# Kernel optimization log

Measured on AMD Instinct MI355X. Metric: run time of the kernel, lower is better.

The kernel has to match this reference:

```python
import jax, jax.numpy as jnp
import numpy as np
from jax import lax

B, C, H, W = 32, 3, 128, 128
S = 10             # max_segments
L = 200            # base_traj_length
TOTAL_LIMIT = 200  # traj_length (must equal L per original sample())
DOF = 2
HID = 2048
CONV_OUT = 512 * 6 * 6  # 128->126->63->61->30->28->14->12->6


def _conv(x, w, b):
    y = lax.conv_general_dilated(x, w, (1, 1), 'VALID', dimension_numbers=('NCHW', 'OIHW', 'NCHW'))
    return y + b[None, :, None, None]


def _pool_relu(x):
    return jax.nn.relu(lax.reduce_window(x, -jnp.inf, lax.max, (1, 1, 2, 2), (1, 1, 2, 2), 'VALID'))


def _rotate2d(y, y0, rot):
    # rotate points y (B,L,2) around per-batch center y0 (B,2) by rot (B,1,1) radians
    px, py = y[..., 0:1], y[..., 1:2]
    cx, cy = y0[:, 0][:, None, None], y0[:, 1][:, None, None]
    c, s = jnp.cos(rot), jnp.sin(rot)
    return jnp.concatenate([c * (px - cx) - s * (py - cy) + cx,
                            s * (px - cx) + c * (py - cy) + cy], axis=2)


def _sample(traj, ratio):
    b, T = traj.shape[0], traj.shape[1]
    f32 = traj.dtype
    seg_limit = jnp.ceil(ratio * TOTAL_LIMIT)  # (B,S)
    # redistribution: shave 1 off the (first) max segment while over budget.
    # original runs over_limit.max() iterations; over_limit <= S-1, extras are no-ops (still_over gate).
    for _ in range(S):
        max_val = seg_limit.max(axis=1)
        still_over = (seg_limit.sum(axis=1) != float(L)).astype(f32)
        reduced = jnp.ones((b,), f32)
        for j in range(S):
            mult = jnp.abs(jnp.sign(max_val - seg_limit[:, j]) - 1.0)
            seg_limit = seg_limit.at[:, j].add(-mult * reduced * still_over)
            reduced = jnp.clip(reduced - mult, 0.0)
    seg_ids = np.arange(T) // L
    # replicates original condition: i>0 and cur_segment_idx != floor(i - 1/L)  (note: i - 1/L, as written)
    forces = np.array([(i > 0) and (seg_ids[i] != int(np.floor(i - 1.0 / L))) for i in range(T)])
    di0 = jnp.floor((L - 1.0) / seg_limit[:, 0:1])
    init = (di0, jnp.zeros((b, 1), f32), jnp.zeros((b, 1), f32), jnp.zeros((b, S), f32))

    def step(state, inp):
        di, last_idx, n_tot, seg_cnt = state
        i_f, seg, force = inp
        lim = lax.dynamic_index_in_dim(seg_limit, seg, axis=1, keepdims=True)  # (B,1)
        cnt = lax.dynamic_index_in_dim(seg_cnt, seg, axis=1, keepdims=True)    # (B,1)
        new_di = jnp.floor((L - 1.0 - (last_idx - seg.astype(f32) * L)) / (lim - cnt))
        di = jnp.where(force | (di < new_di), new_di, di)
        chk = (jnp.sign(jnp.clip(TOTAL_LIMIT - n_tot, 0.0))
               * (cnt < lim).astype(f32)
               * (i_f - last_idx == di).astype(f32))
        last_idx = jnp.maximum(last_idx, i_f * chk)
        seg_cnt = lax.dynamic_update_index_in_dim(seg_cnt, (cnt + chk)[:, 0], seg, axis=1)
        return (di, last_idx, n_tot + chk, seg_cnt), chk[:, 0]

    xs = (jnp.arange(T, dtype=f32), jnp.asarray(seg_ids, jnp.int32), jnp.asarray(forces))
    _, mask_t = lax.scan(step, init, xs)
    mask = mask_t.T > 0  # (B,T) velocity mask; exactly TOTAL_LIMIT true per row
    idx = jnp.argsort(jnp.where(mask, 0, 1), axis=1)[:, :TOTAL_LIMIT]  # stable sort -> ordered true positions
    return jnp.take_along_axis(traj, idx[:, :, None], axis=1)


def _forward(x, w1, b1, w2, b2, w3, b3, w4, b4, fcw1, fcb1, fcw2, fcb2,
             wi, bi, ws, bs, wr, br, base_traj):
    h = _pool_relu(_conv(x, w1, b1))
    h = _pool_relu(_conv(h, w2, b2))
    h = _pool_relu(_conv(h, w3, b3))
    h = _pool_relu(_conv(h, w4, b4))
    feat = h.reshape(h.shape[0], -1)  # (B, CONV_OUT)
    z = jnp.tanh(feat @ fcw1.T + fcb1)
    z = z @ fcw2.T + fcb2             # dropout == identity (eval mode)
    init_pos = z @ wi.T + bi                                   # (B,DOF)
    seg_mod = (z @ ws.T + bs).reshape(z.shape[0], S, DOF + 1)  # (B,S,DOF+1)
    ratio = jax.nn.softmax(z @ wr.T + br, axis=1)              # (B,S)
    last_pos = init_pos[:, None, :]
    starts, segs = [last_pos], []
    for i in range(S):
        scaling = seg_mod[:, i, :-1]
        rot = jnp.tanh(seg_mod[:, i, -1])[:, None, None] * 3.14
        m = base_traj * scaling[:, None, :]
        m = _rotate2d(m, m[:, 0, :], rot)
        m = last_pos + m
        last_pos = m[:, -1:, :]
        starts.append(last_pos)
        segs.append(m)
    traj = jnp.concatenate(segs, axis=1)             # (B,S*L,DOF) unsampled
    seg_start_end = jnp.concatenate(starts, axis=1)  # (B,S+1,DOF)
    sampled = _sample(traj, ratio)                   # (B,TOTAL_LIMIT,DOF)
    return sampled, seg_start_end, ratio, traj


def setup_inputs():
    key = jax.random.key(0)
    ks = jax.random.split(key, 12)
    n = lambda k, s, sc: jax.random.normal(k, s, jnp.float32) * sc
    t = jnp.linspace(0.0, 1.0, L)
    base_traj = jnp.stack([t, jnp.sin(t * jnp.pi)], axis=-1)[None]  # (1,L,2)
    return {
        'x': n(ks[0], (B, C, H, W), 1.0),
        'w1': n(ks[1], (64, C, 3, 3), 0.05), 'b1': jnp.zeros((64,), jnp.float32),
        'w2': n(ks[2], (128, 64, 3, 3), 0.05), 'b2': jnp.zeros((128,), jnp.float32),
        'w3': n(ks[3], (256, 128, 3, 3), 0.05), 'b3': jnp.zeros((256,), jnp.float32),
        'w4': n(ks[4], (512, 256, 3, 3), 0.05), 'b4': jnp.zeros((512,), jnp.float32),
        'fcw1': n(ks[5], (HID, CONV_OUT), 0.01), 'fcb1': jnp.zeros((HID,), jnp.float32),
        'fcw2': n(ks[6], (HID, HID), 0.02), 'fcb2': jnp.zeros((HID,), jnp.float32),
        'wi': n(ks[7], (DOF, HID), 0.02), 'bi': jnp.zeros((DOF,), jnp.float32),
        'ws': n(ks[8], (S * (DOF + 1), HID), 0.02), 'bs': jnp.zeros((S * (DOF + 1),), jnp.float32),
        'wr': n(ks[9], (S, HID), 0.05), 'br': jnp.zeros((S,), jnp.float32),
        'base_traj': base_traj,
    }


def reference(x, w1, b1, w2, b2, w3, b3, w4, b4, fcw1, fcb1, fcw2, fcb2,
              wi, bi, ws, bs, wr, br, base_traj):
    return _forward(x, w1, b1, w2, b2, w3, b3, w4, b4, fcw1, fcb1, fcw2, fcb2,
                    wi, bi, ws, bs, wr, br, base_traj)
```

## Files before the change

kernel.cpp:

```cpp
#include <hip/hip_runtime.h>

__global__ __launch_bounds__(256)
void conv1_lds(const float* __restrict__ in, const float* __restrict__ wt,
               const float* __restrict__ bias, float* __restrict__ out)
{
    __shared__ float sh[3][34][34];
    int bx = blockIdx.x;
    int tile = bx & 15;
    int cg   = (bx >> 4) & 7;
    int b    = bx >> 7;
    int tr = tile >> 2, tc = tile & 3;
    int tid = threadIdx.x;
    int ty = tid >> 4, tx = tid & 15;
    int R0 = 32 * tr, C0 = 32 * tc;

    for (int t = tid; t < 3 * 34 * 34; t += 256) {
        int ci = t / 1156;
        int rem = t - ci * 1156;
        int rr = rem / 34, cc = rem - rr * 34;
        int gr = R0 + rr; if (gr > 127) gr = 127;
        int gc = C0 + cc; if (gc > 127) gc = 127;
        sh[ci][rr][cc] = in[(((size_t)b * 3 + ci) * 128 + gr) * 128 + gc];
    }
    __syncthreads();

    float acc[8][2][2] = {};
    int co0 = cg * 8;
#pragma unroll
    for (int ci = 0; ci < 3; ++ci) {
        float p[4][4];
#pragma unroll
        for (int r = 0; r < 4; ++r) {
            const float2* pr = reinterpret_cast<const float2*>(&sh[ci][2 * ty + r][2 * tx]);
            float2 a = pr[0], c2 = pr[1];
            p[r][0] = a.x; p[r][1] = a.y; p[r][2] = c2.x; p[r][3] = c2.y;
        }
#pragma unroll
        for (int j = 0; j < 8; ++j) {
            const float* wj = wt + ((size_t)(co0 + j) * 3 + ci) * 9;
#pragma unroll
            for (int kh = 0; kh < 3; ++kh)
#pragma unroll
                for (int kw = 0; kw < 3; ++kw) {
                    float wv = wj[kh * 3 + kw];
#pragma unroll
                    for (int dy = 0; dy < 2; ++dy)
#pragma unroll
                        for (int dx = 0; dx < 2; ++dx)
                            acc[j][dy][dx] = fmaf(wv, p[dy + kh][dx + kw], acc[j][dy][dx]);
                }
        }
    }
    int py = 16 * tr + ty, px = 16 * tc + tx;
    if (py < 63 && px < 63) {
#pragma unroll
        for (int j = 0; j < 8; ++j) {
            float v = fmaxf(fmaxf(acc[j][0][0], acc[j][0][1]),
                            fmaxf(acc[j][1][0], acc[j][1][1])) + bias[co0 + j];
            out[(((size_t)b * 64 + co0 + j) * 63 + py) * 63 + px] = fmaxf(v, 0.f);
        }
    }
}

template<int CIN, int DIM, int POOL, int COUT, int TILES_R, int TILES_C>
__global__ __launch_bounds__(256)
void conv_v9(const float* __restrict__ in, const float* __restrict__ wt,
             const float* __restrict__ bias, float* __restrict__ out)
{
    __shared__ __align__(16) float in_sh[2][648];
    __shared__ __align__(16) float w_sh[2][384];

    constexpr int NT  = TILES_R * TILES_C;
    constexpr int NCG = COUT / 32;
    int bx = blockIdx.x;
    int tile = bx % NT;
    int cg   = (bx / NT) % NCG;
    int b    = bx / (NT * NCG);
    int rt = tile / TILES_C, ct = tile % TILES_C;
    int tid = threadIdx.x;
    int co_l = tid & 15;
    int sp   = tid >> 4;
    int ty = sp >> 2, tx = sp & 3;
    int R0 = 16 * rt, C0 = 32 * ct;

    int gofs[3], lofs[3];
#pragma unroll
    for (int j = 0; j < 3; ++j) {
        int t = tid + 256 * j; if (t > 611) t = 611;
        int rr = t / 34, cc = t - rr * 34;
        int gr = R0 + rr; if (gr > DIM - 1) gr = DIM - 1;
        int gc = C0 + cc; if (gc > DIM - 1) gc = DIM - 1;
        gofs[j] = gr * DIM + gc;
        lofs[j] = rr * 36 + cc;
    }
    int wgofs[2], wlofs[2];
#pragma unroll
    for (int j = 0; j < 2; ++j) {
        int t = tid + 256 * j; if (t > 287) t = 287;
        int c = t / 9, k = t - c * 9;
        wgofs[j] = (cg * 32 + c) * CIN * 9 + k;
        wlofs[j] = c * 12 + k;
    }
    bool wv1 = (tid < 32);

    const float* gci = in + (size_t)b * CIN * DIM * DIM;
    const float* wci = wt;

    float acc[2][4][8] = {};
    float sr[3], wr[2];

#pragma unroll
    for (int j = 0; j < 3; ++j) sr[j] = gci[gofs[j]];
    wr[0] = wci[wgofs[0]];
    wr[1] = wci[wgofs[1]];
#pragma unroll
    for (int j = 0; j < 3; ++j) { int t = tid + 256 * j; if (t < 612) in_sh[0][lofs[j]] = sr[j]; }
    w_sh[0][wlofs[0]] = wr[0];
    if (wv1) w_sh[0][wlofs[1]] = wr[1];
    __syncthreads();

    for (int ci = 0; ci < CIN; ++ci) {
        int p = ci & 1;
        if (ci < CIN - 1) {
            const float* gn = gci + (size_t)(ci + 1) * DIM * DIM;
            const float* wn = wci + (size_t)(ci + 1) * 9;
#pragma unroll
            for (int j = 0; j < 3; ++j) sr[j] = gn[gofs[j]];
            wr[0] = wn[wgofs[0]];
            wr[1] = wn[wgofs[1]];
        }
        float w[2][9];
#pragma unroll
        for (int h = 0; h < 2; ++h)
#pragma unroll
            for (int k = 0; k < 9; ++k)
                w[h][k] = w_sh[p][(co_l + 16 * h) * 12 + k];
        const float* rb = in_sh[p] + 8 * tx;
#pragma unroll
        for (int r = 0; r < 6; ++r) {
            const float* rp = rb + (4 * ty + r) * 36;
            float4 a = *reinterpret_cast<const float4*>(rp);
            float4 b4 = *reinterpret_cast<const float4*>(rp + 4);
            float2 c2 = *reinterpret_cast<const float2*>(rp + 8);
            float row[10];
            row[0] = a.x;  row[1] = a.y;  row[2] = a.z;  row[3] = a.w;
            row[4] = b4.x; row[5] = b4.y; row[6] = b4.z; row[7] = b4.w;
            row[8] = c2.x; row[9] = c2.y;
#pragma unroll
            for (int y = 0; y < 4; ++y) {
                if (y < r - 2 || y > r) continue;
                int kh = r - y;
#pragma unroll
                for (int kw = 0; kw < 3; ++kw) {
                    float w0 = w[0][kh * 3 + kw];
                    float w1 = w[1][kh * 3 + kw];
#pragma unroll
                    for (int x = 0; x < 8; ++x) {
                        acc[0][y][x] = fmaf(w0, row[x + kw], acc[0][y][x]);
                        acc[1][y][x] = fmaf(w1, row[x + kw], acc[1][y][x]);
                    }
                }
            }
        }
        if (ci < CIN - 1) {
#pragma unroll
            for (int j = 0; j < 3; ++j) { int t = tid + 256 * j; if (t < 612) in_sh[p ^ 1][lofs[j]] = sr[j]; }
            w_sh[p ^ 1][wlofs[0]] = wr[0];
            if (wv1) w_sh[p ^ 1][wlofs[1]] = wr[1];
        }
        __syncthreads();
    }

#pragma unroll
    for (int h = 0; h < 2; ++h) {
        int co = cg * 32 + co_l + 16 * h;
        float bz = bias[co];
#pragma unroll
        for (int dy = 0; dy < 2; ++dy) {
            int py = 8 * rt + 2 * ty + dy;
#pragma unroll
            for (int dx = 0; dx < 4; ++dx) {
                int px = 16 * ct + 4 * tx + dx;
                if (py < POOL && px < POOL) {
                    float v = fmaxf(fmaxf(acc[h][2 * dy][2 * dx],     acc[h][2 * dy][2 * dx + 1]),
                                    fmaxf(acc[h][2 * dy + 1][2 * dx], acc[h][2 * dy + 1][2 * dx + 1]));
                    out[(((size_t)b * COUT + co) * POOL + py) * POOL + px] = fmaxf(v + bz, 0.f);
                }
            }
        }
    }
}

__global__ __launch_bounds__(256)
void conv4_v3(const float* __restrict__ in, const float* __restrict__ wt,
              const float* __restrict__ bias, float* __restrict__ out)
{
    __shared__ __align__(16) float smem[4032 + 4 * 16 * 37];
    float* in_sh = smem;
    float* w_sh  = smem + 4032;
    float* red   = smem;

    int bx = blockIdx.x;
    int cg = bx & 31;
    int b  = bx >> 5;
    int tid = threadIdx.x;
    int h   = tid >> 6;
    int r6  = tid & 63;
    int cog = r6 >> 3;
    int sub = r6 & 7;
    int R = 3 * (sub >> 1), C = 6 * (sub & 1);

    float acc[2][3][6] = {};
    float sin_r[13];
    float sw_r[9];

    const size_t in_b = (size_t)b * 256 * 196;

#pragma unroll
    for (int j = 0; j < 13; ++j) {
        int g = tid + 256 * j;
        if (g < 3136) {
            int hh = g / 784, rem = g - hh * 784;
            int ci = rem / 196, r2 = rem - ci * 196;
            sin_r[j] = in[in_b + (size_t)(hh * 64 + ci) * 196 + r2];
        }
    }
#pragma unroll
    for (int j = 0; j < 9; ++j) {
        int g = tid + 256 * j;
        int hh = g / 576, rem = g - hh * 576;
        int co = rem / 36, q = rem - co * 36;
        sw_r[j] = wt[(size_t)(cg * 16 + co) * 2304 + (size_t)(hh * 64) * 9 + q];
    }

    for (int it = 0; it < 16; ++it) {
#pragma unroll
        for (int j = 0; j < 13; ++j) {
            int g = tid + 256 * j;
            if (g < 3136) {
                int hh = g / 784, rem = g - hh * 784;
                int ci = rem / 196, r2 = rem - ci * 196;
                int rr = r2 / 14, cc = r2 - rr * 14;
                in_sh[((hh * 4 + ci) * 14 + rr) * 18 + cc] = sin_r[j];
            }
        }
#pragma unroll
        for (int j = 0; j < 9; ++j) {
            int g = tid + 256 * j;
            int hh = g / 576, rem = g - hh * 576;
            int co = rem / 36, q = rem - co * 36;
            w_sh[(hh * 16 + co) * 37 + q] = sw_r[j];
        }
        __syncthreads();
        if (it < 15) {
            int k0n = (it + 1) * 4;
#pragma unroll
            for (int j = 0; j < 13; ++j) {
                int g = tid + 256 * j;
                if (g < 3136) {
                    int hh = g / 784, rem = g - hh * 784;
                    int ci = rem / 196, r2 = rem - ci * 196;
                    sin_r[j] = in[in_b + (size_t)(hh * 64 + k0n + ci) * 196 + r2];
                }
            }
#pragma unroll
            for (int j = 0; j < 9; ++j) {
                int g = tid + 256 * j;
                int hh = g / 576, rem = g - hh * 576;
                int co = rem / 36, q = rem - co * 36;
                sw_r[j] = wt[(size_t)(cg * 16 + co) * 2304 + (size_t)(hh * 64 + k0n) * 9 + q];
            }
        }
#pragma unroll
        for (int ci = 0; ci < 4; ++ci) {
            float w[2][9];
#pragma unroll
            for (int c = 0; c < 2; ++c)
#pragma unroll
                for (int k = 0; k < 9; ++k)
                    w[c][k] = w_sh[(h * 16 + 2 * cog + c) * 37 + ci * 9 + k];
            const float* rowbase = in_sh + ((h * 4 + ci) * 14) * 18;
#pragma unroll
            for (int r = 0; r < 5; ++r) {
                float row[8];
                const float2* pr = reinterpret_cast<const float2*>(rowbase + (size_t)(R + r) * 18 + C);
                float2 a0 = pr[0], a1 = pr[1], a2 = pr[2], a3 = pr[3];
                row[0] = a0.x; row[1] = a0.y; row[2] = a1.x; row[3] = a1.y;
                row[4] = a2.x; row[5] = a2.y; row[6] = a3.x; row[7] = a3.y;
#pragma unroll
                for (int y = 0; y < 3; ++y) {
                    if (y < r - 2 || y > r) continue;
                    int kh = r - y;
#pragma unroll
                    for (int c = 0; c < 2; ++c)
#pragma unroll
                        for (int kw = 0; kw < 3; ++kw) {
                            float wv = w[c][kh * 3 + kw];
#pragma unroll
                            for (int x = 0; x < 6; ++x)
                                acc[c][y][x] = fmaf(wv, row[x + kw], acc[c][y][x]);
                        }
                }
            }
        }
        __syncthreads();
    }
#pragma unroll
    for (int hh = 0; hh < 4; ++hh) {
        if (h == hh) {
#pragma unroll
            for (int c = 0; c < 2; ++c)
#pragma unroll
                for (int y = 0; y < 3; ++y)
#pragma unroll
                    for (int x = 0; x < 6; ++x) {
                        float* dst = &red[((2 * cog + c) * 12 + R + y) * 13 + C + x];
                        if (hh == 0) *dst = acc[c][y][x];
                        else         *dst += acc[c][y][x];
                    }
        }
        __syncthreads();
    }
    for (int t = tid; t < 576; t += 256) {
        int co = t / 36, rem = t - co * 36;
        int pr = rem / 6, pc = rem - pr * 6;
        const float* rp = &red[(co * 12 + 2 * pr) * 13 + 2 * pc];
        float v = fmaxf(fmaxf(rp[0], rp[1]), fmaxf(rp[13], rp[14]));
        v += bias[cg * 16 + co];
        out[(((size_t)b * 512 + cg * 16 + co) * 6 + pr) * 6 + pc] = fmaxf(v, 0.f);
    }
}

__global__ __launch_bounds__(1024)
void fc_big(const float* __restrict__ X, const float* __restrict__ W,
            const float* __restrict__ bias, float* __restrict__ Y,
            int K, int N, int act)
{
    __shared__ float red[32][32][8];
    int o0 = blockIdx.x * 8;
    int s = threadIdx.x & 31;
    int b = threadIdx.x >> 5;
    int K4 = K >> 2;
    const float4* X4 = reinterpret_cast<const float4*>(X) + (size_t)b * K4;
    const float4* W4 = reinterpret_cast<const float4*>(W);

    float acc[8] = {};
    for (int k4 = s; k4 < K4; k4 += 32) {
        float4 xv = X4[k4];
#pragma unroll
        for (int o = 0; o < 8; ++o) {
            float4 wv = W4[(size_t)(o0 + o) * K4 + k4];
            acc[o] = fmaf(xv.x, wv.x,
                     fmaf(xv.y, wv.y,
                     fmaf(xv.z, wv.z,
                     fmaf(xv.w, wv.w, acc[o]))));
        }
    }
#pragma unroll
    for (int o = 0; o < 8; ++o) red[b][s][o] = acc[o];
    __syncthreads();
    if (threadIdx.x < 256) {
        int bb = threadIdx.x >> 3, oo = threadIdx.x & 7;
        float v = bias[o0 + oo];
#pragma unroll 8
        for (int ss = 0; ss < 32; ++ss) v += red[bb][ss][oo];
        if (act) v = tanhf(v);
        Y[(size_t)bb * N + o0 + oo] = v;
    }
}

__global__ __launch_bounds__(256)
void fc_two(const float* __restrict__ X, const float* __restrict__ W,
            const float* __restrict__ bias, float* __restrict__ Y,
            int K, int N, int act)
{
    int o0 = blockIdx.x * 2;
    int tid = threadIdx.x;
    const float* w0 = W + (size_t)o0 * K;
    const float* w1 = w0 + K;
    float a0[32], a1[32];
#pragma unroll
    for (int b = 0; b < 32; ++b) { a0[b] = 0.f; a1[b] = 0.f; }

    for (int k = tid; k < K; k += 256) {
        float wv0 = w0[k], wv1 = w1[k];
#pragma unroll
        for (int b = 0; b < 32; ++b) {
            float xv = X[(size_t)b * K + k];
            a0[b] = fmaf(wv0, xv, a0[b]);
            a1[b] = fmaf(wv1, xv, a1[b]);
        }
    }
    __shared__ float part[2][4][32];
    int lane = tid & 63, wv = tid >> 6;
#pragma unroll
    for (int b = 0; b < 32; ++b) {
        float s0 = a0[b], s1 = a1[b];
#pragma unroll
        for (int off = 32; off >= 1; off >>= 1) {
            s0 += __shfl_down(s0, off);
            s1 += __shfl_down(s1, off);
        }
        if (lane == 0) { part[0][wv][b] = s0; part[1][wv][b] = s1; }
    }
    __syncthreads();
    if (tid < 64) {
        int j = tid >> 5, b = tid & 31;
        float s = part[j][0][b] + part[j][1][b] + part[j][2][b] + part[j][3][b] + bias[o0 + j];
        if (act) s = tanhf(s);
        Y[(size_t)b * N + o0 + j] = s;
    }
}

__global__ __launch_bounds__(64)
void post_kernel(const float* __restrict__ logits, float* __restrict__ ratio_out,
                 float* __restrict__ sl_out)
{
    int b = threadIdx.x;
    if (b >= 32) return;
    float lg[10];
#pragma unroll
    for (int j = 0; j < 10; ++j) lg[j] = logits[b * 10 + j];
    float mx = lg[0];
#pragma unroll
    for (int j = 1; j < 10; ++j) mx = fmaxf(mx, lg[j]);
    float e[10]; float ssum = 0.f;
#pragma unroll
    for (int j = 0; j < 10; ++j) { e[j] = expf(lg[j] - mx); ssum += e[j]; }
    float sl[10];
#pragma unroll
    for (int j = 0; j < 10; ++j) {
        float r = e[j] / ssum;
        ratio_out[b * 10 + j] = r;
        sl[j] = ceilf(r * 200.f);
    }
#pragma unroll
    for (int it = 0; it < 10; ++it) {
        float s = 0.f, mx2 = sl[0];
#pragma unroll
        for (int j = 0; j < 10; ++j) { s += sl[j]; mx2 = fmaxf(mx2, sl[j]); }
        float over = (s != 200.f) ? 1.f : 0.f;
        float reduced = 1.f;
#pragma unroll
        for (int j = 0; j < 10; ++j) {
            float mult = (sl[j] == mx2) ? 1.f : 0.f;
            sl[j] -= mult * reduced * over;
            reduced = fmaxf(reduced - mult, 0.f);
        }
    }
#pragma unroll
    for (int j = 0; j < 10; ++j) sl_out[b * 10 + j] = sl[j];
}

__global__ __launch_bounds__(256)
void traj_kernel(const float* __restrict__ base, const float* __restrict__ ipos,
                 const float* __restrict__ sm, float* __restrict__ out_traj,
                 float* __restrict__ out_starts)
{
    int b = blockIdx.x;
    int j = threadIdx.x;
    float bx0 = base[0], by0 = base[1];
    float bxL = base[398], byL = base[399];
    float bx = 0.f, by = 0.f;
    if (j < 200) { bx = base[2 * j]; by = base[2 * j + 1]; }
    float curx = ipos[b * 2 + 0], cury = ipos[b * 2 + 1];
    if (j == 0) { out_starts[b * 22 + 0] = curx; out_starts[b * 22 + 1] = cury; }
#pragma unroll
    for (int i = 0; i < 10; ++i) {
        float sx  = sm[b * 30 + i * 3 + 0];
        float sy  = sm[b * 30 + i * 3 + 1];
        float rot = tanhf(sm[b * 30 + i * 3 + 2]) * 3.14f;
        float c = cosf(rot), s = sinf(rot);
        float cx = bx0 * sx, cy = by0 * sy;
        if (j < 200) {
            float px = bx * sx, py = by * sy;
            float rx = c * (px - cx) - s * (py - cy) + cx;
            float ry = s * (px - cx) + c * (py - cy) + cy;
            size_t o = ((size_t)b * 2000 + i * 200 + j) * 2;
            out_traj[o + 0] = curx + rx;
            out_traj[o + 1] = cury + ry;
        }
        float pxL = bxL * sx, pyL = byL * sy;
        float exL = c * (pxL - cx) - s * (pyL - cy) + cx;
        float eyL = s * (pxL - cx) + c * (pyL - cy) + cy;
        curx += exL; cury += eyL;
        if (j == 0) {
            out_starts[b * 22 + (i + 1) * 2 + 0] = curx;
            out_starts[b * 22 + (i + 1) * 2 + 1] = cury;
        }
    }
}

__global__ __launch_bounds__(64)
void sample_kernel(const float* __restrict__ sl_in, const float* __restrict__ traj,
                   float* __restrict__ samp_out)
{
    __shared__ unsigned int maskb[32][63];
    __shared__ float ssl[32][10];
    int tid = threadIdx.x;
    for (int t = tid; t < 32 * 63; t += 64) ((unsigned int*)maskb)[t] = 0u;
    for (int t = tid; t < 32 * 10; t += 64) ((float*)ssl)[t] = sl_in[t];
    __syncthreads();
    if (tid >= 32) return;
    int b = tid;
    const float* tb = traj + (size_t)b * 4000;
    float* sp = samp_out + (size_t)b * 400;
    int out_n = 0;
    float last = 0.f, ntot = 0.f;
    float lim0 = ssl[b][0];
    float di = floorf(199.f / lim0);
    float ct0 = 0.f;
    if ((ntot < 200.f) && (ct0 < lim0) && (0.f - last == di)) {
        ntot += 1.f; ct0 += 1.f;
        maskb[b][0] |= 1u;
        sp[out_n * 2] = tb[0]; sp[out_n * 2 + 1] = tb[1]; ++out_n;
    }
    {
        float ndi = floorf((199.f - last) / (lim0 - ct0));
        if (di < ndi) di = ndi;
        if ((ntot < 200.f) && (ct0 < lim0) && (1.f - last == di)) {
            last = 1.f; ntot += 1.f; ct0 += 1.f;
            maskb[b][0] |= 2u;
            sp[out_n * 2] = tb[2]; sp[out_n * 2 + 1] = tb[3]; ++out_n;
        }
    }
    for (int seg = 0; seg < 10; ++seg) {
        float lim = ssl[b][seg];
        float ct = (seg == 0) ? ct0 : 0.f;
        float segbase = 200.f * seg;
        float segend = segbase + 199.f;
        float pos = (seg == 0) ? 2.f : segbase;
        float ndi = floorf((199.f - (last - segbase)) / (lim - ct));
        while ((ntot < 200.f) && (ct < lim)) {
            float fi = last + ndi;
            if (!(fi >= pos && fi <= segend)) break;
            int i = (int)fi;
            last = fi; ntot += 1.f; ct += 1.f;
            maskb[b][i >> 5] |= (1u << (i & 31));
            sp[out_n * 2] = tb[2 * i]; sp[out_n * 2 + 1] = tb[2 * i + 1]; ++out_n;
            pos = fi + 1.f;
            ndi = floorf((199.f - (last - segbase)) / (lim - ct));
        }
    }
    for (int i = 0; i < 2000 && out_n < 200; ++i) {
        if (!((maskb[b][i >> 5] >> (i & 31)) & 1u)) {
            sp[out_n * 2] = tb[2 * i]; sp[out_n * 2 + 1] = tb[2 * i + 1]; ++out_n;
        }
    }
}

extern "C" void kernel_launch(void* const* d_in, const int* in_sizes, int n_in,
                              void* d_out, int out_size, void* d_ws, size_t ws_size,
                              hipStream_t stream)
{
    const float* x    = (const float*)d_in[0];
    const float* w1   = (const float*)d_in[1];
    const float* b1   = (const float*)d_in[2];
    const float* w2   = (const float*)d_in[3];
    const float* b2   = (const float*)d_in[4];
    const float* w3   = (const float*)d_in[5];
    const float* b3   = (const float*)d_in[6];
    const float* w4   = (const float*)d_in[7];
    const float* b4   = (const float*)d_in[8];
    const float* fcw1 = (const float*)d_in[9];
    const float* fcb1 = (const float*)d_in[10];
    const float* fcw2 = (const float*)d_in[11];
    const float* fcb2 = (const float*)d_in[12];
    const float* wi   = (const float*)d_in[13];
    const float* bi   = (const float*)d_in[14];
    const float* wsw  = (const float*)d_in[15];
    const float* bs   = (const float*)d_in[16];
    const float* wr   = (const float*)d_in[17];
    const float* br   = (const float*)d_in[18];
    const float* base = (const float*)d_in[19];

    float* out = (float*)d_out;
    float* ws  = (float*)d_ws;

    float* p1   = ws + 0;
    float* p2   = ws + 8128512;
    float* p3   = ws + 0;
    float* feat = ws + 8128512;
    float* z1   = ws + 0;
    float* z2   = ws + 65536;
    float* ipos = ws + 131072;
    float* smod = ws + 131136;
    float* rlog = ws + 132096;
    float* slim = ws + 132416;

    float* out_samp   = out;
    float* out_starts = out + 12800;
    float* out_ratio  = out + 13504;
    float* out_traj   = out + 13824;

    conv1_lds<<<4096, 256, 0, stream>>>(x, w1, b1, p1);
    conv_v9<64, 63, 30, 128, 4, 2><<<1024, 256, 0, stream>>>(p1, w2, b2, p2);
    conv_v9<128, 30, 14, 256, 2, 1><<<512, 256, 0, stream>>>(p2, w3, b3, p3);
    conv4_v3<<<1024, 256, 0, stream>>>(p3, w4, b4, feat);

    fc_big<<<256, 1024, 0, stream>>>(feat, fcw1, fcb1, z1, 18432, 2048, 1);
    fc_big<<<256, 1024, 0, stream>>>(z1, fcw2, fcb2, z2, 2048, 2048, 0);

    fc_two<<<1, 256, 0, stream>>>(z2, wi, bi, ipos, 2048, 2, 0);
    fc_two<<<15, 256, 0, stream>>>(z2, wsw, bs, smod, 2048, 30, 0);
    fc_two<<<5, 256, 0, stream>>>(z2, wr, br, rlog, 2048, 10, 0);

    post_kernel<<<1, 64, 0, stream>>>(rlog, out_ratio, slim);
    traj_kernel<<<32, 256, 0, stream>>>(base, ipos, smod, out_traj, out_starts);
    sample_kernel<<<1, 64, 0, stream>>>(slim, out_traj, out_samp);
}
```

Before: 975.2 us.

## Add specialized conv3 kernel with smaller spatial tiles and double-buffered LDS

Replaces the generic templated conv3 launch with a dedicated kernel. It uses 16x16 output tiles over 32 output channels per block, which doubles the grid from 512 to 1024 blocks. Input-channel slices and weights are double-buffered in LDS, with register prefetch of the next channel overlapping compute. The goal is better occupancy and hidden global-load latency, at the cost of one barrier per input channel and some redundant halo loads.

```diff
diff --git a/kernel.cpp b/kernel.cpp
--- a/kernel.cpp
+++ b/kernel.cpp
@@ -185,6 +185,130 @@
                     float v = fmaxf(fmaxf(acc[h][2 * dy][2 * dx],     acc[h][2 * dy][2 * dx + 1]),
                                     fmaxf(acc[h][2 * dy + 1][2 * dx], acc[h][2 * dy + 1][2 * dx + 1]));
                     out[(((size_t)b * COUT + co) * POOL + py) * POOL + px] = fmaxf(v + bz, 0.f);
+                }
+            }
+        }
+    }
+}
+
+__global__ __launch_bounds__(256)
+void conv3_v10(const float* __restrict__ in, const float* __restrict__ wt,
+               const float* __restrict__ bias, float* __restrict__ out)
+{
+    __shared__ __align__(16) float in_sh[2][360];
+    __shared__ __align__(16) float w_sh[2][384];
+
+    int bx = blockIdx.x;
+    int tile = bx & 3;
+    int cg   = (bx >> 2) & 7;
+    int b    = bx >> 5;
+    int rt = tile >> 1, ct = tile & 1;
+    int tid = threadIdx.x;
+    int co_l = tid & 15;
+    int sp   = tid >> 4;
+    int ty = sp >> 2, tx = sp & 3;
+    int R0 = 16 * rt, C0 = 16 * ct;
+
+    int gofs[2];
+#pragma unroll
+    for (int j = 0; j < 2; ++j) {
+        int t = tid + 256 * j; if (t > 359) t = 359;
+        int rr = t / 20, cc = t - rr * 20;
+        int gr = R0 + rr; if (gr > 29) gr = 29;
+        int gc = C0 + cc; if (gc > 29) gc = 29;
+        gofs[j] = gr * 30 + gc;
+    }
+    int lo1 = (tid + 256 > 359) ? 359 : tid + 256;
+    int wgofs[2], wlofs[2];
+#pragma unroll
+    for (int j = 0; j < 2; ++j) {
+        int t = tid + 256 * j; if (t > 287) t = 287;
+        int c = t / 9, k = t - c * 9;
+        wgofs[j] = (cg * 32 + c) * 128 * 9 + k;
+        wlofs[j] = c * 12 + k;
+    }
+    bool wv1 = (tid < 32);
+
+    const float* gci = in + (size_t)b * 128 * 900;
+    const float* wci = wt;
+
+    float acc[2][4][4] = {};
+    float sr[2], wr[2];
+
+    sr[0] = gci[gofs[0]];
+    sr[1] = gci[gofs[1]];
+    wr[0] = wci[wgofs[0]];
+    wr[1] = wci[wgofs[1]];
+    in_sh[0][tid] = sr[0];
+    if (tid < 104) in_sh[0][lo1] = sr[1];
+    w_sh[0][wlofs[0]] = wr[0];
+    if (wv1) w_sh[0][wlofs[1]] = wr[1];
+    __syncthreads();
+
+    for (int ci = 0; ci < 128; ++ci) {
+        int p = ci & 1;
+        if (ci < 127) {
+            const float* gn = gci + (size_t)(ci + 1) * 900;
+            const float* wn = wci + (size_t)(ci + 1) * 9;
+            sr[0] = gn[gofs[0]];
+            sr[1] = gn[gofs[1]];
+            wr[0] = wn[wgofs[0]];
+            wr[1] = wn[wgofs[1]];
+        }
+        float w[2][9];
+#pragma unroll
+        for (int h = 0; h < 2; ++h)
+#pragma unroll
+            for (int k = 0; k < 9; ++k)
+                w[h][k] = w_sh[p][(co_l + 16 * h) * 12 + k];
+        const float* rb = in_sh[p] + 4 * tx;
+#pragma unroll
+        for (int r = 0; r < 6; ++r) {
+            const float* rp = rb + (4 * ty + r) * 20;
+            float4 a = *reinterpret_cast<const float4*>(rp);
+            float2 c2 = *reinterpret_cast<const float2*>(rp + 4);
+            float row[6];
+            row[0] = a.x; row[1] = a.y; row[2] = a.z; row[3] = a.w;
+            row[4] = c2.x; row[5] = c2.y;
+#pragma unroll
+            for (int y = 0; y < 4; ++y) {
+                if (y < r - 2 || y > r) continue;
+                int kh = r - y;
+#pragma unroll
+                for (int kw = 0; kw < 3; ++kw) {
+                    float w0 = w[0][kh * 3 + kw];
+                    float w1 = w[1][kh * 3 + kw];
+#pragma unroll
+                    for (int x = 0; x < 4; ++x) {
+                        acc[0][y][x] = fmaf(w0, row[x + kw], acc[0][y][x]);
+                        acc[1][y][x] = fmaf(w1, row[x + kw], acc[1][y][x]);
+                    }
+                }
+            }
+        }
+        if (ci < 127) {
+            in_sh[p ^ 1][tid] = sr[0];
+            if (tid < 104) in_sh[p ^ 1][lo1] = sr[1];
+            w_sh[p ^ 1][wlofs[0]] = wr[0];
+            if (wv1) w_sh[p ^ 1][wlofs[1]] = wr[1];
+        }
+        __syncthreads();
+    }
+
+#pragma unroll
+    for (int h = 0; h < 2; ++h) {
+        int co = cg * 32 + co_l + 16 * h;
+        float bz = bias[co];
+#pragma unroll
+        for (int dy = 0; dy < 2; ++dy) {
+            int py = 8 * rt + 2 * ty + dy;
+#pragma unroll
+            for (int dx = 0; dx < 2; ++dx) {
+                int px = 8 * ct + 2 * tx + dx;
+                if (py < 14 && px < 14) {
+                    float v = fmaxf(fmaxf(acc[h][2 * dy][2 * dx],     acc[h][2 * dy][2 * dx + 1]),
+                                    fmaxf(acc[h][2 * dy + 1][2 * dx], acc[h][2 * dy + 1][2 * dx + 1]));
+                    out[(((size_t)b * 256 + co) * 14 + py) * 14 + px] = fmaxf(v + bz, 0.f);
                 }
             }
         }
@@ -595,7 +719,7 @@
 
     conv1_lds<<<4096, 256, 0, stream>>>(x, w1, b1, p1);
     conv_v9<64, 63, 30, 128, 4, 2><<<1024, 256, 0, stream>>>(p1, w2, b2, p2);
-    conv_v9<128, 30, 14, 256, 2, 1><<<512, 256, 0, stream>>>(p2, w3, b3, p3);
+    conv3_v10<<<1024, 256, 0, stream>>>(p2, w3, b3, p3);
     conv4_v3<<<1024, 256, 0, stream>>>(p3, w4, b4, feat);
 
     fc_big<<<256, 1024, 0, stream>>>(feat, fcw1, fcb1, z1, 18432, 2048, 1);
```

Measured after the change: 1.001 ms. 2.6% more time.
